# Performance work log

Measured on AMD Instinct MI355X. Metric: run time of the kernel, lower is better.

Reference implementation:

```python
import jax, jax.numpy as jnp
import numpy as np

NX = 2048
NL = 20
BATCH = 512
EIGMAX = 10.0
EPS = 1e-9


def prox_cardan(eta, x):
    """Prox of u -> -eta*(log(u)+log(1-u)) at x: unique root in (0,1) of
    u^3 - (1+x)u^2 + (x-2eta)u + eta = 0 (Cardano / trigonometric method)."""
    b = -(1.0 + x)
    c = x - 2.0 * eta
    d = eta
    p = c - b * b / 3.0
    q = 2.0 * b ** 3 / 27.0 - b * c / 3.0 + d
    disc = -4.0 * p ** 3 - 27.0 * q ** 2
    # three-real-roots branch (trigonometric); requires p<0
    pm = jnp.minimum(p, -1e-12)
    m = 2.0 * jnp.sqrt(-pm / 3.0)
    arg = jnp.clip(3.0 * q / (pm * m), -1.0, 1.0)
    th = jnp.arccos(arg)
    k = jnp.arange(3, dtype=x.dtype)
    t_trig = m[..., None] * jnp.cos((th[..., None] - 2.0 * jnp.pi * k) / 3.0)
    r_trig = t_trig - b[..., None] / 3.0
    in01 = (r_trig > 0.0) & (r_trig < 1.0)
    idx = jnp.argmax(in01, axis=-1)
    root3 = jnp.take_along_axis(r_trig, idx[..., None], axis=-1)[..., 0]
    # one-real-root branch
    s = jnp.sqrt(jnp.maximum(q * q / 4.0 + p ** 3 / 27.0, 0.0))
    root1 = jnp.cbrt(-q / 2.0 + s) + jnp.cbrt(-q / 2.0 - s) - b / 3.0
    u = jnp.where(disc >= 0.0, root3, root1)
    return jnp.clip(u, EPS, 1.0 - EPS)


def setup_inputs() -> dict:
    key = jax.random.key(0)
    k1, k2, k3, k4, k5 = jax.random.split(key, 5)
    x = jax.random.uniform(k1, (BATCH, 1, NX), dtype=jnp.float32)
    # symmetric PSD operators for T^T T and D^T D (as in a discretized inverse problem)
    A = jax.random.normal(k2, (NX, NX), dtype=jnp.float32)
    tTT = (A @ A.T) / NX
    B = jax.random.normal(k3, (NX, NX), dtype=jnp.float32)
    tDD = (B @ B.T) / NX
    # orthogonal change-of-basis: element <-> eigen bases
    Q, _ = jnp.linalg.qr(jax.random.normal(k4, (NX, NX), dtype=jnp.float32))
    Pelt = Q.astype(jnp.float32)
    Peig = Q.T.astype(jnp.float32)
    x_b = jnp.einsum('ij,bcj->bci', tTT, x) + 0.01 * jax.random.normal(k5, (BATCH, 1, NX), dtype=jnp.float32)
    gamma = jnp.full((NL,), 0.1, dtype=jnp.float32)   # nn.Parameter([0.1])
    mu = jnp.zeros((NL,), dtype=jnp.float32)          # nn.Parameter([0.0])
    reg = jnp.full((NL,), 0.001, dtype=jnp.float32)   # noisy=True -> trainable 0.001
    return {"x": x, "x_b": x_b, "tDD": tDD, "tTT": tTT, "Peig": Peig,
            "Pelt": Pelt, "gamma": gamma, "mu": mu, "reg": reg}


def reference(x, x_b, tDD, tTT, Peig, Pelt, gamma, mu, reg):
    def step(xc, params):
        g_raw, mu_raw, reg_raw = params
        g = jax.nn.softplus(g_raw)
        mu_l = jax.nn.softplus(mu_raw) / 1e6
        reg_l = jax.nn.softplus(reg_raw) / (EIGMAX ** 2)
        grad = (jnp.einsum('ij,bcj->bci', tTT, xc) - x_b
                + reg_l * jnp.einsum('ij,bcj->bci', tDD, xc))
        xt = xc - g * grad
        xt = jnp.einsum('ij,bcj->bci', Pelt, xt)
        xt = prox_cardan(g * mu_l, xt)
        xt = jnp.einsum('ij,bcj->bci', Peig, xt)
        return xt, None

    out, _ = jax.lax.scan(step, x, (gamma, mu, reg))
    return out
```

## Files before the change

### kernel.cpp

```cpp
#include <hip/hip_runtime.h>
#include <math.h>

#define MDIM 512
#define NDIM 2048
#define KDIM 2048
#define NLAYERS 20

static const size_t MN = (size_t)MDIM * NDIM;
static const size_t OPN = (size_t)KDIM * KDIM;

using bf16x8 = __attribute__((ext_vector_type(8))) short;
using f32x4  = __attribute__((ext_vector_type(4))) float;

__device__ __forceinline__ double softplusd(double v) {
    return (v > 20.0) ? v : log1p(exp(v));
}

__device__ __forceinline__ float prox_cardan_f(float eta, float x) {
    const float b  = -(1.0f + x);
    const float c  = x - 2.0f * eta;
    const float dd = eta;
    const float p  = c - b * b * (1.0f / 3.0f);
    const float q  = 2.0f * b * b * b * (1.0f / 27.0f) - b * c * (1.0f / 3.0f) + dd;
    const float disc = -4.0f * p * p * p - 27.0f * q * q;
    const float pm = fminf(p, -1e-12f);
    const float mm = 2.0f * sqrtf(-pm * (1.0f / 3.0f));
    float arg = 3.0f * q / (pm * mm);
    arg = fminf(fmaxf(arg, -1.0f), 1.0f);
    const float th = acosf(arg);
    const float TWO_PI = 6.28318530717958647692f;
    const float r0 = mm * cosf(th * (1.0f / 3.0f)) - b * (1.0f / 3.0f);
    const float r1 = mm * cosf((th - TWO_PI) * (1.0f / 3.0f)) - b * (1.0f / 3.0f);
    const float r2 = mm * cosf((th - 2.0f * TWO_PI) * (1.0f / 3.0f)) - b * (1.0f / 3.0f);
    const bool in0 = (r0 > 0.0f) && (r0 < 1.0f);
    const bool in1 = (r1 > 0.0f) && (r1 < 1.0f);
    const bool in2 = (r2 > 0.0f) && (r2 < 1.0f);
    const float root3 = in0 ? r0 : (in1 ? r1 : (in2 ? r2 : r0));
    const float s = sqrtf(fmaxf(q * q * 0.25f + p * p * p * (1.0f / 27.0f), 0.0f));
    const float root1 = cbrtf(-q * 0.5f + s) + cbrtf(-q * 0.5f - s) - b * (1.0f / 3.0f);
    const float u = (disc >= 0.0f) ? root3 : root1;
    return fminf(fmaxf(u, 1e-9f), 1.0f - 1e-9f);
}

__device__ __forceinline__ double prox_newton_d(double eta, double x) {
    double u = (double)prox_cardan_f((float)eta, (float)x);
#pragma unroll
    for (int i = 0; i < 4; ++i) {
        const double um1 = u - 1.0;
        const double umx = u - x;
        const double P  = u * um1 * umx - eta * (2.0 * u - 1.0);
        const double dP = um1 * umx + u * umx + u * um1 - 2.0 * eta;
        u = u - P / dP;
        u = fmin(fmax(u, 1e-12), 1.0 - 1e-12);
    }
    return fmin(fmax(u, 1e-9), 1.0 - 1e-9);
}

__device__ __forceinline__ unsigned short f2bf(float f) {
    unsigned u = __float_as_uint(f);
    unsigned r = (u + 0x7FFFu + ((u >> 16) & 1u)) >> 16;
    return (unsigned short)r;
}
__device__ __forceinline__ float bf2f(unsigned short h) {
    return __uint_as_float(((unsigned)h) << 16);
}
__device__ __forceinline__ void split3f(float f, unsigned short& b1,
                                        unsigned short& b2, unsigned short& b3) {
    b1 = f2bf(f);
    const float r1 = f - bf2f(b1);
    b2 = f2bf(r1);
    const float r2 = r1 - bf2f(b2);
    b3 = f2bf(r2);
}

__device__ __forceinline__ void gl16(const void* g, void* l) {
    __builtin_amdgcn_global_load_lds(
        (const __attribute__((address_space(1))) unsigned int*)g,
        (__attribute__((address_space(3))) unsigned int*)l, 16, 0, 0);
}

__global__ __launch_bounds__(256) void split3_op(
    const float* __restrict__ s1, const float* __restrict__ s2,
    const float* __restrict__ greg, int layer,
    unsigned short* __restrict__ p1, unsigned short* __restrict__ p2,
    unsigned short* __restrict__ p3) {
    const size_t i = ((size_t)blockIdx.x * 256 + threadIdx.x) * 4;
    float reglf = 0.0f;
    if (s2) reglf = (float)(softplusd((double)greg[layer]) * 0.01);
    const float4 a = *(const float4*)(s1 + i);
    float4 b = make_float4(0.f, 0.f, 0.f, 0.f);
    if (s2) b = *(const float4*)(s2 + i);
    ushort4 o1, o2, o3;
    split3f(fmaf(reglf, b.x, a.x), o1.x, o2.x, o3.x);
    split3f(fmaf(reglf, b.y, a.y), o1.y, o2.y, o3.y);
    split3f(fmaf(reglf, b.z, a.z), o1.z, o2.z, o3.z);
    split3f(fmaf(reglf, b.w, a.w), o1.w, o2.w, o3.w);
    *(ushort4*)(p1 + i) = o1;
    *(ushort4*)(p2 + i) = o2;
    *(ushort4*)(p3 + i) = o3;
}

__global__ __launch_bounds__(256) void split3_w(
    const float* __restrict__ s1, const float* __restrict__ s2,
    const float* __restrict__ greg, int layer,
    unsigned short* __restrict__ p1, unsigned short* __restrict__ p2,
    unsigned short* __restrict__ p3) {
    if (layer > 0 && greg[layer] == greg[0]) return;
    const size_t i = ((size_t)blockIdx.x * 256 + threadIdx.x) * 4;
    const float reglf = (float)(softplusd((double)greg[layer]) * 0.01);
    const float4 a = *(const float4*)(s1 + i);
    const float4 b = *(const float4*)(s2 + i);
    ushort4 o1, o2, o3;
    split3f(fmaf(reglf, b.x, a.x), o1.x, o2.x, o3.x);
    split3f(fmaf(reglf, b.y, a.y), o1.y, o2.y, o3.y);
    split3f(fmaf(reglf, b.z, a.z), o1.z, o2.z, o3.z);
    split3f(fmaf(reglf, b.w, a.w), o1.w, o2.w, o3.w);
    *(ushort4*)(p1 + i) = o1;
    *(ushort4*)(p2 + i) = o2;
    *(ushort4*)(p3 + i) = o3;
}

__global__ __launch_bounds__(256, 2) void gemm_bf16x3(
    const unsigned short* __restrict__ A1, const unsigned short* __restrict__ A2,
    const unsigned short* __restrict__ A3,
    const unsigned short* __restrict__ W1, const unsigned short* __restrict__ W2,
    const unsigned short* __restrict__ W3,
    float* __restrict__ Part, int klen, int S) {
    __shared__ __align__(16) unsigned short Ab[3][3][64][32];
    __shared__ __align__(16) unsigned short Wb[3][3][64][32];

    const int tid = threadIdx.x;

    const int nwg = 256 * S;
    const int cpx = nwg >> 3;
    const int bid = blockIdx.x;
    const int g   = (bid & 7) * cpx + (bid >> 3);
    const int xs  = g / (8 * S);
    const int rr  = g - xs * (8 * S);
    const int ys  = rr & 7;
    const int zs  = rr >> 3;
    const int n0 = xs * 64;
    const int m0 = ys * 64;
    const int kb = zs * klen;

    const int lane = tid & 63, wid = tid >> 6;
    const int quad = lane >> 4, lrow = lane & 15;
    const int wm = (wid >> 1) * 32, wn = (wid & 1) * 32;

    const int srow = tid >> 2;
    const int lc8  = ((tid & 3) ^ ((tid >> 3) & 3)) * 8;
    const int t8   = tid * 8;
    const int qx   = (quad ^ ((lrow >> 1) & 3)) * 8;

    const unsigned short* gA1 = A1 + (size_t)(m0 + srow) * KDIM + kb + lc8;
    const unsigned short* gA2 = A2 + (size_t)(m0 + srow) * KDIM + kb + lc8;
    const unsigned short* gA3 = A3 + (size_t)(m0 + srow) * KDIM + kb + lc8;
    const unsigned short* gW1 = W1 + (size_t)(n0 + srow) * KDIM + kb + lc8;
    const unsigned short* gW2 = W2 + (size_t)(n0 + srow) * KDIM + kb + lc8;
    const unsigned short* gW3 = W3 + (size_t)(n0 + srow) * KDIM + kb + lc8;

    unsigned short* lA = &Ab[0][0][0][0];
    unsigned short* lW = &Wb[0][0][0][0];

    f32x4 ahi[2][2], alo[2][2];
#pragma unroll
    for (int a = 0; a < 2; ++a)
#pragma unroll
        for (int b = 0; b < 2; ++b) {
            ahi[a][b] = (f32x4){0.f, 0.f, 0.f, 0.f};
            alo[a][b] = (f32x4){0.f, 0.f, 0.f, 0.f};
        }

    auto stage = [&](int buf, int step) {
        const int off = buf * 6144;
        const int ko  = step * 32;
        gl16(gA1 + ko, lA + off + t8);
        gl16(gA2 + ko, lA + off + 2048 + t8);
        gl16(gA3 + ko, lA + off + 4096 + t8);
        gl16(gW1 + ko, lW + off + t8);
        gl16(gW2 + ko, lW + off + 2048 + t8);
        gl16(gW3 + ko, lW + off + 4096 + t8);
    };

    const int nsteps = klen >> 5;

    stage(0, 0);
    if (nsteps > 1) stage(1, 1);

    int idx = 0;
    for (int s = 0; s < nsteps; ++s) {
        if (s + 1 < nsteps) {
            asm volatile("s_waitcnt vmcnt(6)" ::: "memory");
        } else {
            asm volatile("s_waitcnt vmcnt(0)" ::: "memory");
        }
        __builtin_amdgcn_s_barrier();
        __builtin_amdgcn_sched_barrier(0);

        if (s + 2 < nsteps) {
            int pre = idx + 2; if (pre >= 3) pre -= 3;
            stage(pre, s + 2);
        }

        const unsigned short* cA = lA + idx * 6144;
        const unsigned short* cW = lW + idx * 6144;

        bf16x8 fa[2][3], fw[2][3];
#pragma unroll
        for (int t = 0; t < 2; ++t) {
            const int ra = (wm + t * 16 + lrow) * 32;
            const int rw = (wn + t * 16 + lrow) * 32;
            fa[t][0] = *(const bf16x8*)(cA + ra + qx);
            fa[t][1] = *(const bf16x8*)(cA + 2048 + ra + qx);
            fa[t][2] = *(const bf16x8*)(cA + 4096 + ra + qx);
            fw[t][0] = *(const bf16x8*)(cW + rw + qx);
            fw[t][1] = *(const bf16x8*)(cW + 2048 + rw + qx);
            fw[t][2] = *(const bf16x8*)(cW + 4096 + rw + qx);
        }
        __builtin_amdgcn_s_setprio(1);
#pragma unroll
        for (int tm = 0; tm < 2; ++tm)
#pragma unroll
            for (int tn = 0; tn < 2; ++tn) {
                ahi[tm][tn] = __builtin_amdgcn_mfma_f32_16x16x32_bf16(fa[tm][0], fw[tn][0], ahi[tm][tn], 0, 0, 0);
                alo[tm][tn] = __builtin_amdgcn_mfma_f32_16x16x32_bf16(fa[tm][0], fw[tn][1], alo[tm][tn], 0, 0, 0);
                alo[tm][tn] = __builtin_amdgcn_mfma_f32_16x16x32_bf16(fa[tm][1], fw[tn][0], alo[tm][tn], 0, 0, 0);
                alo[tm][tn] = __builtin_amdgcn_mfma_f32_16x16x32_bf16(fa[tm][1], fw[tn][1], alo[tm][tn], 0, 0, 0);
                alo[tm][tn] = __builtin_amdgcn_mfma_f32_16x16x32_bf16(fa[tm][0], fw[tn][2], alo[tm][tn], 0, 0, 0);
                alo[tm][tn] = __builtin_amdgcn_mfma_f32_16x16x32_bf16(fa[tm][2], fw[tn][0], alo[tm][tn], 0, 0, 0);
            }
        __builtin_amdgcn_s_setprio(0);

        ++idx; if (idx == 3) idx = 0;
    }

    float* P = Part + (size_t)zs * MN;
#pragma unroll
    for (int tm = 0; tm < 2; ++tm)
#pragma unroll
        for (int tn = 0; tn < 2; ++tn) {
            const int mbase = m0 + wm + tm * 16 + quad * 4;
            const int nn = n0 + wn + tn * 16 + lrow;
#pragma unroll
            for (int r = 0; r < 4; ++r)
                P[(size_t)(mbase + r) * NDIM + nn] = ahi[tm][tn][r] + alo[tm][tn][r];
        }
}

template <int MODE>
__global__ __launch_bounds__(256) void combine3(
    const float* __restrict__ Part, int S,
    const float* __restrict__ Xc, const float* __restrict__ Xb,
    float* __restrict__ stateOut,
    unsigned short* __restrict__ p1, unsigned short* __restrict__ p2,
    unsigned short* __restrict__ p3,
    const float* __restrict__ gam, const float* __restrict__ gmu,
    const float* __restrict__ greg, int layer) {
    const size_t i = ((size_t)blockIdx.x * 256 + threadIdx.x) * 4;
    double s0 = 0.0, s1 = 0.0, s2 = 0.0, s3 = 0.0;
    for (int z = 0; z < S; ++z) {
        const float4 p = *(const float4*)(Part + (size_t)z * MN + i);
        s0 += (double)p.x; s1 += (double)p.y; s2 += (double)p.z; s3 += (double)p.w;
    }
    float v0, v1, v2, v3;
    if (MODE == 0) {
        const double g = softplusd((double)gam[layer]);
        const float4 xc = *(const float4*)(Xc + i);
        const float4 xb = *(const float4*)(Xb + i);
        v0 = (float)((double)xc.x - g * (s0 - (double)xb.x));
        v1 = (float)((double)xc.y - g * (s1 - (double)xb.y));
        v2 = (float)((double)xc.z - g * (s2 - (double)xb.z));
        v3 = (float)((double)xc.w - g * (s3 - (double)xb.w));
    } else if (MODE == 1) {
        const double g   = softplusd((double)gam[layer]);
        const double eta = g * softplusd((double)gmu[layer]) * 1e-6;
        v0 = (float)prox_newton_d(eta, s0);
        v1 = (float)prox_newton_d(eta, s1);
        v2 = (float)prox_newton_d(eta, s2);
        v3 = (float)prox_newton_d(eta, s3);
    } else {
        v0 = (float)s0; v1 = (float)s1; v2 = (float)s2; v3 = (float)s3;
        *(float4*)(stateOut + i) = make_float4(v0, v1, v2, v3);
    }
    ushort4 o1, o2, o3;
    split3f(v0, o1.x, o2.x, o3.x);
    split3f(v1, o1.y, o2.y, o3.y);
    split3f(v2, o1.z, o2.z, o3.z);
    split3f(v3, o1.w, o2.w, o3.w);
    *(ushort4*)(p1 + i) = o1;
    *(ushort4*)(p2 + i) = o2;
    *(ushort4*)(p3 + i) = o3;
}

#define BM 64
#define BN 64
#define BK 32
#define LDSP 68

__device__ __forceinline__ double prox_cardan_d(double eta, double x) {
    const double b  = -(1.0 + x);
    const double c  = x - 2.0 * eta;
    const double dd = eta;
    const double p  = c - b * b * (1.0 / 3.0);
    const double q  = 2.0 * b * b * b * (1.0 / 27.0) - b * c * (1.0 / 3.0) + dd;
    const double disc = -4.0 * p * p * p - 27.0 * q * q;
    const double pm = fmin(p, -1e-12);
    const double mm = 2.0 * sqrt(-pm * (1.0 / 3.0));
    double arg = 3.0 * q / (pm * mm);
    arg = fmin(fmax(arg, -1.0), 1.0);
    const double th = acos(arg);
    const double TWO_PI = 6.283185307179586476925286766559;
    const double r0 = mm * cos(th * (1.0 / 3.0)) - b * (1.0 / 3.0);
    const double r1 = mm * cos((th - TWO_PI) * (1.0 / 3.0)) - b * (1.0 / 3.0);
    const double r2 = mm * cos((th - 2.0 * TWO_PI) * (1.0 / 3.0)) - b * (1.0 / 3.0);
    const bool in0 = (r0 > 0.0) && (r0 < 1.0);
    const bool in1 = (r1 > 0.0) && (r1 < 1.0);
    const bool in2 = (r2 > 0.0) && (r2 < 1.0);
    const double root3 = in0 ? r0 : (in1 ? r1 : (in2 ? r2 : r0));
    const double s = sqrt(fmax(q * q * 0.25 + p * p * p * (1.0 / 27.0), 0.0));
    const double root1 = cbrt(-q * 0.5 + s) + cbrt(-q * 0.5 - s) - b * (1.0 / 3.0);
    const double u = (disc >= 0.0) ? root3 : root1;
    return fmin(fmax(u, 1e-9), 1.0 - 1e-9);
}

template <bool FUSE2>
__global__ __launch_bounds__(256, 4) void gemm_nt_splitk(
    const float* __restrict__ A, const float* __restrict__ W1,
    const float* __restrict__ W2, double* __restrict__ Part,
    const float* __restrict__ greg, int layer, int klen) {
    __shared__ float As[BK][LDSP];
    __shared__ float Ws[BK][LDSP];
    const int tid = threadIdx.x;
    const int m0 = blockIdx.y * BM;
    const int n0 = blockIdx.x * BN;
    const int kbase = blockIdx.z * klen;
    float reglf = 0.0f;
    if (FUSE2) reglf = (float)(softplusd((double)greg[layer]) * 0.01);
    const int lrow = tid >> 3;
    const int lkc  = (tid & 7) << 2;
    const float* pA  = A  + (size_t)(m0 + lrow) * KDIM + kbase + lkc;
    const float* pW  = W1 + (size_t)(n0 + lrow) * KDIM + kbase + lkc;
    const float* pW2 = FUSE2 ? (W2 + (size_t)(n0 + lrow) * KDIM + kbase + lkc) : nullptr;
    float4 ra[2], rw[2];
    ra[0] = *(const float4*)(pA);
    ra[1] = *(const float4*)(pA + 32 * KDIM);
    rw[0] = *(const float4*)(pW);
    rw[1] = *(const float4*)(pW + 32 * KDIM);
    if (FUSE2) {
        const float4 u0 = *(const float4*)(pW2);
        const float4 u1 = *(const float4*)(pW2 + 32 * KDIM);
        rw[0].x += reglf * u0.x; rw[0].y += reglf * u0.y;
        rw[0].z += reglf * u0.z; rw[0].w += reglf * u0.w;
        rw[1].x += reglf * u1.x; rw[1].y += reglf * u1.y;
        rw[1].z += reglf * u1.z; rw[1].w += reglf * u1.w;
    }
    float  acc[4][4]   = {};
    double acc64[4][4] = {};
    const int tx = (tid & 15) << 2;
    const int ty = (tid >> 4) << 2;
    int it = 0;
    for (int k0 = 0; k0 < klen; k0 += BK, ++it) {
#pragma unroll
        for (int h = 0; h < 2; ++h) {
            const int row = lrow + (h << 5);
            As[lkc + 0][row] = (h ? ra[1].x : ra[0].x);
            As[lkc + 1][row] = (h ? ra[1].y : ra[0].y);
            As[lkc + 2][row] = (h ? ra[1].z : ra[0].z);
            As[lkc + 3][row] = (h ? ra[1].w : ra[0].w);
            Ws[lkc + 0][row] = (h ? rw[1].x : rw[0].x);
            Ws[lkc + 1][row] = (h ? rw[1].y : rw[0].y);
            Ws[lkc + 2][row] = (h ? rw[1].z : rw[0].z);
            Ws[lkc + 3][row] = (h ? rw[1].w : rw[0].w);
        }
        __syncthreads();
        if (k0 + BK < klen) {
            const float* qA = pA + k0 + BK;
            ra[0] = *(const float4*)(qA);
            ra[1] = *(const float4*)(qA + 32 * KDIM);
            const float* qW = pW + k0 + BK;
            rw[0] = *(const float4*)(qW);
            rw[1] = *(const float4*)(qW + 32 * KDIM);
            if (FUSE2) {
                const float* qW2 = pW2 + k0 + BK;
                const float4 u0 = *(const float4*)(qW2);
                const float4 u1 = *(const float4*)(qW2 + 32 * KDIM);
                rw[0].x += reglf * u0.x; rw[0].y += reglf * u0.y;
                rw[0].z += reglf * u0.z; rw[0].w += reglf * u0.w;
                rw[1].x += reglf * u1.x; rw[1].y += reglf * u1.y;
                rw[1].z += reglf * u1.z; rw[1].w += reglf * u1.w;
            }
        }
#pragma unroll
        for (int kk = 0; kk < BK; ++kk) {
            const float4 a4 = *(const float4*)(&As[kk][ty]);
            const float4 b4 = *(const float4*)(&Ws[kk][tx]);
            const float av[4] = {a4.x, a4.y, a4.z, a4.w};
            const float bv[4] = {b4.x, b4.y, b4.z, b4.w};
#pragma unroll
            for (int r = 0; r < 4; ++r)
#pragma unroll
                for (int cc = 0; cc < 4; ++cc)
                    acc[r][cc] = fmaf(av[r], bv[cc], acc[r][cc]);
        }
        __syncthreads();
        if ((it & 1) == 1) {
#pragma unroll
            for (int r = 0; r < 4; ++r)
#pragma unroll
                for (int cc = 0; cc < 4; ++cc) {
                    acc64[r][cc] += (double)acc[r][cc];
                    acc[r][cc] = 0.0f;
                }
        }
    }
#pragma unroll
    for (int r = 0; r < 4; ++r)
#pragma unroll
        for (int cc = 0; cc < 4; ++cc)
            acc64[r][cc] += (double)acc[r][cc];
    double* Pz = Part + (size_t)blockIdx.z * MN;
#pragma unroll
    for (int r = 0; r < 4; ++r) {
        double* q = Pz + (size_t)(m0 + ty + r) * NDIM + n0 + tx;
        *(double2*)(q)     = make_double2(acc64[r][0], acc64[r][1]);
        *(double2*)(q + 2) = make_double2(acc64[r][2], acc64[r][3]);
    }
}

template <int MODE>
__global__ __launch_bounds__(256) void combine_ep(
    const double* __restrict__ Part, int nslices,
    const float* __restrict__ Xc, const float* __restrict__ Xb,
    float* __restrict__ Out,
    const float* __restrict__ gam, const float* __restrict__ gmu,
    const float* __restrict__ greg, int layer) {
    const size_t i4 = ((size_t)blockIdx.x * 256 + threadIdx.x) * 4;
    double s0 = 0.0, s1 = 0.0, s2 = 0.0, s3 = 0.0;
    for (int z = 0; z < nslices; ++z) {
        const double* p = Part + (size_t)z * MN + i4;
        const double2 a = *(const double2*)(p);
        const double2 b = *(const double2*)(p + 2);
        s0 += a.x; s1 += a.y; s2 += b.x; s3 += b.y;
    }
    float4 o;
    if (MODE == 0) {
        const double g = softplusd((double)gam[layer]);
        const float4 xc = *(const float4*)(Xc + i4);
        const float4 xb = *(const float4*)(Xb + i4);
        o.x = (float)((double)xc.x - g * (s0 - (double)xb.x));
        o.y = (float)((double)xc.y - g * (s1 - (double)xb.y));
        o.z = (float)((double)xc.z - g * (s2 - (double)xb.z));
        o.w = (float)((double)xc.w - g * (s3 - (double)xb.w));
    } else if (MODE == 1) {
        const double g   = softplusd((double)gam[layer]);
        const double eta = g * softplusd((double)gmu[layer]) * 1e-6;
        o.x = (float)prox_cardan_d(eta, s0);
        o.y = (float)prox_cardan_d(eta, s1);
        o.z = (float)prox_cardan_d(eta, s2);
        o.w = (float)prox_cardan_d(eta, s3);
    } else {
        o.x = (float)s0; o.y = (float)s1; o.z = (float)s2; o.w = (float)s3;
    }
    *(float4*)(Out + i4) = o;
}

extern "C" void kernel_launch(void* const* d_in, const int* in_sizes, int n_in,
                              void* d_out, int out_size, void* d_ws, size_t ws_size,
                              hipStream_t stream) {
    const float* x    = (const float*)d_in[0];
    const float* x_b  = (const float*)d_in[1];
    const float* tDD  = (const float*)d_in[2];
    const float* tTT  = (const float*)d_in[3];
    const float* Peig = (const float*)d_in[4];
    const float* Pelt = (const float*)d_in[5];
    const float* gam  = (const float*)d_in[6];
    const float* gmu  = (const float*)d_in[7];
    const float* greg = (const float*)d_in[8];
    float* out = (float*)d_out;

    const size_t TRI_OP_B = 3 * OPN * 2;
    const size_t TRI_A_B  = 3 * MN * 2;
    const size_t STATE_B  = MN * 4;
    const size_t full_need = 3 * TRI_OP_B + 2 * TRI_A_B + STATE_B + 2 * MN * 4;
    const size_t mid_need  = 1 * TRI_OP_B + 2 * TRI_A_B + STATE_B + 2 * MN * 4;

    const bool full = (ws_size >= full_need);
    const bool mid  = (!full && ws_size >= mid_need);

    if (full || mid) {
        const int S = 2;
        const int klen = KDIM / S;
        char* p = (char*)d_ws;
        unsigned short *Wt1, *Wt2, *Wt3, *Pe1, *Pe2, *Pe3, *Pg1, *Pg2, *Pg3;
        if (full) {
            Wt1 = (unsigned short*)p;        Wt2 = Wt1 + OPN; Wt3 = Wt2 + OPN; p += TRI_OP_B;
            Pe1 = (unsigned short*)p;        Pe2 = Pe1 + OPN; Pe3 = Pe2 + OPN; p += TRI_OP_B;
            Pg1 = (unsigned short*)p;        Pg2 = Pg1 + OPN; Pg3 = Pg2 + OPN; p += TRI_OP_B;
        } else {
            Wt1 = (unsigned short*)p;        Wt2 = Wt1 + OPN; Wt3 = Wt2 + OPN; p += TRI_OP_B;
            Pe1 = Wt1; Pe2 = Wt2; Pe3 = Wt3;
            Pg1 = Wt1; Pg2 = Wt2; Pg3 = Wt3;
        }
        unsigned short* Aa1 = (unsigned short*)p; unsigned short* Aa2 = Aa1 + MN;
        unsigned short* Aa3 = Aa2 + MN; p += TRI_A_B;
        unsigned short* Ab1 = (unsigned short*)p; unsigned short* Ab2 = Ab1 + MN;
        unsigned short* Ab3 = Ab2 + MN; p += TRI_A_B;
        float* state = (float*)p; p += STATE_B;
        float* part  = (float*)p;

        const dim3 gg((unsigned)(256 * S));
        const unsigned cgrid = (unsigned)(MN / 4 / 256);
        const unsigned ogrid = (unsigned)(OPN / 4 / 256);

        split3_op<<<cgrid, 256, 0, stream>>>(x, nullptr, greg, 0, Aa1, Aa2, Aa3);
        if (full) {
            split3_op<<<ogrid, 256, 0, stream>>>(Pelt, nullptr, greg, 0, Pe1, Pe2, Pe3);
            split3_op<<<ogrid, 256, 0, stream>>>(Peig, nullptr, greg, 0, Pg1, Pg2, Pg3);
        }

        unsigned short *c1 = Aa1, *c2 = Aa2, *c3 = Aa3;
        unsigned short *d1 = Ab1, *d2 = Ab2, *d3 = Ab3;

        for (int l = 0; l < NLAYERS; ++l) {
            if (full) {
                split3_w<<<ogrid, 256, 0, stream>>>(tTT, tDD, greg, l, Wt1, Wt2, Wt3);
            } else {
                split3_op<<<ogrid, 256, 0, stream>>>(tTT, tDD, greg, l, Wt1, Wt2, Wt3);
            }
            gemm_bf16x3<<<gg, 256, 0, stream>>>(c1, c2, c3, Wt1, Wt2, Wt3, part, klen, S);
            combine3<0><<<cgrid, 256, 0, stream>>>(part, S, (l == 0 ? x : state), x_b,
                                                   nullptr, d1, d2, d3, gam, gmu, greg, l);
            if (mid) split3_op<<<ogrid, 256, 0, stream>>>(Pelt, nullptr, greg, 0, Pe1, Pe2, Pe3);
            gemm_bf16x3<<<gg, 256, 0, stream>>>(d1, d2, d3, Pe1, Pe2, Pe3, part, klen, S);
            combine3<1><<<cgrid, 256, 0, stream>>>(part, S, nullptr, nullptr,
                                                   nullptr, c1, c2, c3, gam, gmu, greg, l);
            if (mid) split3_op<<<ogrid, 256, 0, stream>>>(Peig, nullptr, greg, 0, Pg1, Pg2, Pg3);
            gemm_bf16x3<<<gg, 256, 0, stream>>>(c1, c2, c3, Pg1, Pg2, Pg3, part, klen, S);
            combine3<2><<<cgrid, 256, 0, stream>>>(part, S, nullptr, nullptr,
                                                   (l == NLAYERS - 1 ? out : state),
                                                   d1, d2, d3, gam, gmu, greg, l);
            unsigned short* t;
            t = c1; c1 = d1; d1 = t;
            t = c2; c2 = d2; d2 = t;
            t = c3; c3 = d3; d3 = t;
        }
        return;
    }

    char* wsb = (char*)d_ws;
    float* b0 = (float*)wsb;
    float* b1 = b0 + MN;
    float* b2 = b1 + MN;
    float* b3 = b2 + MN;
    const size_t base_bytes = 4 * MN * sizeof(float);
    double* partd = (double*)(wsb + base_bytes);
    int S = 0;
    if (ws_size >= base_bytes + 2 * MN * sizeof(double)) S = 2;
    else if (ws_size >= base_bytes + 1 * MN * sizeof(double)) S = 1;
    if (S == 0) return;
    const int klen = KDIM / S;
    dim3 gg(NDIM / BN, MDIM / BM, S);
    dim3 cg((unsigned)(MN / 4 / 256));
    const float* cur = x;
    float* bx = b0; float* bu = b1; float* bn = b2; float* bo = b3;
    for (int l = 0; l < NLAYERS; ++l) {
        gemm_nt_splitk<true><<<gg, 256, 0, stream>>>(cur, tTT, tDD, partd, greg, l, klen);
        combine_ep<0><<<cg, 256, 0, stream>>>(partd, S, cur, x_b, bx, gam, gmu, greg, l);
        gemm_nt_splitk<false><<<gg, 256, 0, stream>>>(bx, Pelt, nullptr, partd, greg, l, klen);
        combine_ep<1><<<cg, 256, 0, stream>>>(partd, S, nullptr, nullptr, bu, gam, gmu, greg, l);
        gemm_nt_splitk<false><<<gg, 256, 0, stream>>>(bu, Peig, nullptr, partd, greg, l, klen);
        float* dst = (l == NLAYERS - 1) ? out : bn;
        combine_ep<2><<<cg, 256, 0, stream>>>(partd, S, nullptr, nullptr, dst, gam, gmu, greg, l);
        cur = bn;
        float* t = bn; bn = bo; bo = t;
    }
}
```

Measured before the change: 2.719 ms.

## Pre-tile activations into MFMA fragment layout and load A directly to registers

The activation split kernels and combine kernels now write the bf16x3 activation pieces in a fragment-tiled layout matching the MFMA operand order. The GEMM then loads A fragments straight from global memory into registers, double-buffered across steps, instead of staging them through LDS. Each wave stages only its own W rows into a per-wave LDS buffer, which removes the block-wide barrier. The MFMA issue order is also regrouped by component. This cuts LDS traffic and synchronisation but makes each wave rely on global-load latency hiding for A, and it duplicates A fetches across the two waves sharing an m-tile.

Result: slower. 3.026 ms (+11.3%).

```diff
diff --git a/kernel.cpp b/kernel.cpp
--- a/kernel.cpp
+++ b/kernel.cpp
@@ -79,6 +79,7 @@
         (__attribute__((address_space(3))) unsigned int*)l, 16, 0, 0);
 }
 
+
 __global__ __launch_bounds__(256) void split3_op(
     const float* __restrict__ s1, const float* __restrict__ s2,
     const float* __restrict__ greg, int layer,
@@ -120,14 +121,38 @@
     *(ushort4*)(p3 + i) = o3;
 }
 
+__global__ __launch_bounds__(256) void split3_a(
+    const float* __restrict__ src,
+    unsigned short* __restrict__ p1, unsigned short* __restrict__ p2,
+    unsigned short* __restrict__ p3) {
+    const int b = blockIdx.x;
+    const int wid = threadIdx.x >> 6, lane = threadIdx.x & 63;
+    const int msub = b >> 4, kblk = (b & 15) * 4 + wid;
+    const int m = msub * 16 + (lane & 15);
+    const int n = kblk * 32 + (lane >> 4) * 8;
+    const size_t flat = (size_t)m * NDIM + n;
+    const size_t tile = ((size_t)(msub * 64 + kblk) * 64 + lane) * 8;
+    const float4 a = *(const float4*)(src + flat);
+    const float4 c = *(const float4*)(src + flat + 4);
+    const float v[8] = {a.x, a.y, a.z, a.w, c.x, c.y, c.z, c.w};
+    unsigned short o1[8], o2[8], o3[8];
+#pragma unroll
+    for (int j = 0; j < 8; ++j) split3f(v[j], o1[j], o2[j], o3[j]);
+    *(ushort4*)(p1 + tile)     = make_ushort4(o1[0], o1[1], o1[2], o1[3]);
+    *(ushort4*)(p1 + tile + 4) = make_ushort4(o1[4], o1[5], o1[6], o1[7]);
+    *(ushort4*)(p2 + tile)     = make_ushort4(o2[0], o2[1], o2[2], o2[3]);
+    *(ushort4*)(p2 + tile + 4) = make_ushort4(o2[4], o2[5], o2[6], o2[7]);
+    *(ushort4*)(p3 + tile)     = make_ushort4(o3[0], o3[1], o3[2], o3[3]);
+    *(ushort4*)(p3 + tile + 4) = make_ushort4(o3[4], o3[5], o3[6], o3[7]);
+}
+
 __global__ __launch_bounds__(256, 2) void gemm_bf16x3(
     const unsigned short* __restrict__ A1, const unsigned short* __restrict__ A2,
     const unsigned short* __restrict__ A3,
     const unsigned short* __restrict__ W1, const unsigned short* __restrict__ W2,
     const unsigned short* __restrict__ W3,
     float* __restrict__ Part, int klen, int S) {
-    __shared__ __align__(16) unsigned short Ab[3][3][64][32];
-    __shared__ __align__(16) unsigned short Wb[3][3][64][32];
+    __shared__ __align__(16) unsigned short Wb[4][3][3][1024];
 
     const int tid = threadIdx.x;
 
@@ -140,100 +165,131 @@
     const int ys  = rr & 7;
     const int zs  = rr >> 3;
     const int n0 = xs * 64;
-    const int m0 = ys * 64;
     const int kb = zs * klen;
 
     const int lane = tid & 63, wid = tid >> 6;
     const int quad = lane >> 4, lrow = lane & 15;
     const int wm = (wid >> 1) * 32, wn = (wid & 1) * 32;
-
-    const int srow = tid >> 2;
-    const int lc8  = ((tid & 3) ^ ((tid >> 3) & 3)) * 8;
-    const int t8   = tid * 8;
-    const int qx   = (quad ^ ((lrow >> 1) & 3)) * 8;
-
-    const unsigned short* gA1 = A1 + (size_t)(m0 + srow) * KDIM + kb + lc8;
-    const unsigned short* gA2 = A2 + (size_t)(m0 + srow) * KDIM + kb + lc8;
-    const unsigned short* gA3 = A3 + (size_t)(m0 + srow) * KDIM + kb + lc8;
-    const unsigned short* gW1 = W1 + (size_t)(n0 + srow) * KDIM + kb + lc8;
-    const unsigned short* gW2 = W2 + (size_t)(n0 + srow) * KDIM + kb + lc8;
-    const unsigned short* gW3 = W3 + (size_t)(n0 + srow) * KDIM + kb + lc8;
-
-    unsigned short* lA = &Ab[0][0][0][0];
-    unsigned short* lW = &Wb[0][0][0][0];
+    const int swq = (quad ^ ((lrow >> 1) & 3)) * 8;
+
+    const int nsteps = klen >> 5;
+    const int kblk0  = zs * nsteps;
+
+    const unsigned short* pAb[2][3];
+#pragma unroll
+    for (int t = 0; t < 2; ++t) {
+        const int msubA = ys * 4 + (wid >> 1) * 2 + t;
+        const size_t base = ((size_t)(msubA * 64 + kblk0) * 64 + lane) * 8;
+        pAb[t][0] = A1 + base;
+        pAb[t][1] = A2 + base;
+        pAb[t][2] = A3 + base;
+    }
+
+    const int lc8 = ((lane & 3) ^ ((lane >> 3) & 3)) * 8;
+    const size_t wrow = (size_t)(n0 + wn + (lane >> 2)) * KDIM + kb + lc8;
+    const unsigned short* gWs[3] = {W1 + wrow, W2 + wrow, W3 + wrow};
+
+    unsigned short* wbase = &Wb[wid][0][0][0];
 
     f32x4 ahi[2][2], alo[2][2];
 #pragma unroll
     for (int a = 0; a < 2; ++a)
 #pragma unroll
-        for (int b = 0; b < 2; ++b) {
-            ahi[a][b] = (f32x4){0.f, 0.f, 0.f, 0.f};
-            alo[a][b] = (f32x4){0.f, 0.f, 0.f, 0.f};
-        }
-
-    auto stage = [&](int buf, int step) {
-        const int off = buf * 6144;
-        const int ko  = step * 32;
-        gl16(gA1 + ko, lA + off + t8);
-        gl16(gA2 + ko, lA + off + 2048 + t8);
-        gl16(gA3 + ko, lA + off + 4096 + t8);
-        gl16(gW1 + ko, lW + off + t8);
-        gl16(gW2 + ko, lW + off + 2048 + t8);
-        gl16(gW3 + ko, lW + off + 4096 + t8);
-    };
-
-    const int nsteps = klen >> 5;
-
-    stage(0, 0);
-    if (nsteps > 1) stage(1, 1);
-
-    int idx = 0;
-    for (int s = 0; s < nsteps; ++s) {
+        for (int b2 = 0; b2 < 2; ++b2) {
+            ahi[a][b2] = (f32x4){0.f, 0.f, 0.f, 0.f};
+            alo[a][b2] = (f32x4){0.f, 0.f, 0.f, 0.f};
+        }
+
+    bf16x8 faA[2][3], faB[2][3];
+
+#pragma unroll
+    for (int st = 0; st < 2; ++st)
+#pragma unroll
+        for (int p = 0; p < 3; ++p)
+#pragma unroll
+            for (int h = 0; h < 2; ++h)
+                gl16(gWs[p] + (size_t)h * 32768 + st * 32,
+                     wbase + st * 3072 + p * 1024 + h * 512);
+#pragma unroll
+    for (int t = 0; t < 2; ++t)
+#pragma unroll
+        for (int p = 0; p < 3; ++p)
+            faA[t][p] = *(const bf16x8*)(pAb[t][p]);
+    asm volatile("s_waitcnt vmcnt(0)" ::: "memory");
+    __builtin_amdgcn_sched_barrier(0);
+
+    auto STEP = [&](bf16x8 (&cur)[2][3], bf16x8 (&nxt)[2][3], int s) {
         if (s + 1 < nsteps) {
             asm volatile("s_waitcnt vmcnt(6)" ::: "memory");
         } else {
             asm volatile("s_waitcnt vmcnt(0)" ::: "memory");
         }
-        __builtin_amdgcn_s_barrier();
         __builtin_amdgcn_sched_barrier(0);
-
+        if (s + 1 < nsteps) {
+#pragma unroll
+            for (int t = 0; t < 2; ++t)
+#pragma unroll
+                for (int p = 0; p < 3; ++p)
+                    nxt[t][p] = *(const bf16x8*)(pAb[t][p] + (size_t)(s + 1) * 512);
+        }
         if (s + 2 < nsteps) {
-            int pre = idx + 2; if (pre >= 3) pre -= 3;
-            stage(pre, s + 2);
-        }
-
-        const unsigned short* cA = lA + idx * 6144;
-        const unsigned short* cW = lW + idx * 6144;
-
-        bf16x8 fa[2][3], fw[2][3];
+            const int bu = (s + 2) % 3;
+#pragma unroll
+            for (int p = 0; p < 3; ++p)
+#pragma unroll
+                for (int h = 0; h < 2; ++h)
+                    gl16(gWs[p] + (size_t)h * 32768 + (s + 2) * 32,
+                         wbase + bu * 3072 + p * 1024 + h * 512);
+        }
+        const int bc = s % 3;
+        bf16x8 fw[2][3];
 #pragma unroll
         for (int t = 0; t < 2; ++t) {
-            const int ra = (wm + t * 16 + lrow) * 32;
-            const int rw = (wn + t * 16 + lrow) * 32;
-            fa[t][0] = *(const bf16x8*)(cA + ra + qx);
-            fa[t][1] = *(const bf16x8*)(cA + 2048 + ra + qx);
-            fa[t][2] = *(const bf16x8*)(cA + 4096 + ra + qx);
-            fw[t][0] = *(const bf16x8*)(cW + rw + qx);
-            fw[t][1] = *(const bf16x8*)(cW + 2048 + rw + qx);
-            fw[t][2] = *(const bf16x8*)(cW + 4096 + rw + qx);
+            const int roff = (t * 16 + lrow) * 32 + swq;
+#pragma unroll
+            for (int p = 0; p < 3; ++p)
+                fw[t][p] = *(const bf16x8*)(wbase + bc * 3072 + p * 1024 + roff);
         }
         __builtin_amdgcn_s_setprio(1);
 #pragma unroll
         for (int tm = 0; tm < 2; ++tm)
 #pragma unroll
-            for (int tn = 0; tn < 2; ++tn) {
-                ahi[tm][tn] = __builtin_amdgcn_mfma_f32_16x16x32_bf16(fa[tm][0], fw[tn][0], ahi[tm][tn], 0, 0, 0);
-                alo[tm][tn] = __builtin_amdgcn_mfma_f32_16x16x32_bf16(fa[tm][0], fw[tn][1], alo[tm][tn], 0, 0, 0);
-                alo[tm][tn] = __builtin_amdgcn_mfma_f32_16x16x32_bf16(fa[tm][1], fw[tn][0], alo[tm][tn], 0, 0, 0);
-                alo[tm][tn] = __builtin_amdgcn_mfma_f32_16x16x32_bf16(fa[tm][1], fw[tn][1], alo[tm][tn], 0, 0, 0);
-                alo[tm][tn] = __builtin_amdgcn_mfma_f32_16x16x32_bf16(fa[tm][0], fw[tn][2], alo[tm][tn], 0, 0, 0);
-                alo[tm][tn] = __builtin_amdgcn_mfma_f32_16x16x32_bf16(fa[tm][2], fw[tn][0], alo[tm][tn], 0, 0, 0);
-            }
+            for (int tn = 0; tn < 2; ++tn)
+                ahi[tm][tn] = __builtin_amdgcn_mfma_f32_16x16x32_bf16(cur[tm][0], fw[tn][0], ahi[tm][tn], 0, 0, 0);
+#pragma unroll
+        for (int tm = 0; tm < 2; ++tm)
+#pragma unroll
+            for (int tn = 0; tn < 2; ++tn)
+                alo[tm][tn] = __builtin_amdgcn_mfma_f32_16x16x32_bf16(cur[tm][0], fw[tn][1], alo[tm][tn], 0, 0, 0);
+#pragma unroll
+        for (int tm = 0; tm < 2; ++tm)
+#pragma unroll
+            for (int tn = 0; tn < 2; ++tn)
+                alo[tm][tn] = __builtin_amdgcn_mfma_f32_16x16x32_bf16(cur[tm][1], fw[tn][0], alo[tm][tn], 0, 0, 0);
+#pragma unroll
+        for (int tm = 0; tm < 2; ++tm)
+#pragma unroll
+            for (int tn = 0; tn < 2; ++tn)
+                alo[tm][tn] = __builtin_amdgcn_mfma_f32_16x16x32_bf16(cur[tm][1], fw[tn][1], alo[tm][tn], 0, 0, 0);
+#pragma unroll
+        for (int tm = 0; tm < 2; ++tm)
+#pragma unroll
+            for (int tn = 0; tn < 2; ++tn)
+                alo[tm][tn] = __builtin_amdgcn_mfma_f32_16x16x32_bf16(cur[tm][0], fw[tn][2], alo[tm][tn], 0, 0, 0);
+#pragma unroll
+        for (int tm = 0; tm < 2; ++tm)
+#pragma unroll
+            for (int tn = 0; tn < 2; ++tn)
+                alo[tm][tn] = __builtin_amdgcn_mfma_f32_16x16x32_bf16(cur[tm][2], fw[tn][0], alo[tm][tn], 0, 0, 0);
         __builtin_amdgcn_s_setprio(0);
-
-        ++idx; if (idx == 3) idx = 0;
-    }
-
+    };
+
+    for (int s = 0; s < nsteps; s += 2) {
+        STEP(faA, faB, s);
+        STEP(faB, faA, s + 1);
+    }
+
+    const int m0 = ys * 64;
     float* P = Part + (size_t)zs * MN;
 #pragma unroll
     for (int tm = 0; tm < 2; ++tm)
@@ -256,40 +312,54 @@
     unsigned short* __restrict__ p3,
     const float* __restrict__ gam, const float* __restrict__ gmu,
     const float* __restrict__ greg, int layer) {
-    const size_t i = ((size_t)blockIdx.x * 256 + threadIdx.x) * 4;
-    double s0 = 0.0, s1 = 0.0, s2 = 0.0, s3 = 0.0;
+    const int b = blockIdx.x;
+    const int wid = threadIdx.x >> 6, lane = threadIdx.x & 63;
+    const int msub = b >> 4, kblk = (b & 15) * 4 + wid;
+    const int m = msub * 16 + (lane & 15);
+    const int n = kblk * 32 + (lane >> 4) * 8;
+    const size_t flat = (size_t)m * NDIM + n;
+    const size_t tile = ((size_t)(msub * 64 + kblk) * 64 + lane) * 8;
+
+    double s[8] = {0., 0., 0., 0., 0., 0., 0., 0.};
     for (int z = 0; z < S; ++z) {
-        const float4 p = *(const float4*)(Part + (size_t)z * MN + i);
-        s0 += (double)p.x; s1 += (double)p.y; s2 += (double)p.z; s3 += (double)p.w;
-    }
-    float v0, v1, v2, v3;
+        const float4 a = *(const float4*)(Part + (size_t)z * MN + flat);
+        const float4 c = *(const float4*)(Part + (size_t)z * MN + flat + 4);
+        s[0] += (double)a.x; s[1] += (double)a.y; s[2] += (double)a.z; s[3] += (double)a.w;
+        s[4] += (double)c.x; s[5] += (double)c.y; s[6] += (double)c.z; s[7] += (double)c.w;
+    }
+    float v[8];
     if (MODE == 0) {
         const double g = softplusd((double)gam[layer]);
-        const float4 xc = *(const float4*)(Xc + i);
-        const float4 xb = *(const float4*)(Xb + i);
-        v0 = (float)((double)xc.x - g * (s0 - (double)xb.x));
-        v1 = (float)((double)xc.y - g * (s1 - (double)xb.y));
-        v2 = (float)((double)xc.z - g * (s2 - (double)xb.z));
-        v3 = (float)((double)xc.w - g * (s3 - (double)xb.w));
+        const float4 xa = *(const float4*)(Xc + flat);
+        const float4 xc = *(const float4*)(Xc + flat + 4);
+        const float4 ba = *(const float4*)(Xb + flat);
+        const float4 bc = *(const float4*)(Xb + flat + 4);
+        const float xcv[8] = {xa.x, xa.y, xa.z, xa.w, xc.x, xc.y, xc.z, xc.w};
+        const float xbv[8] = {ba.x, ba.y, ba.z, ba.w, bc.x, bc.y, bc.z, bc.w};
+#pragma unroll
+        for (int j = 0; j < 8; ++j)
+            v[j] = (float)((double)xcv[j] - g * (s[j] - (double)xbv[j]));
     } else if (MODE == 1) {
         const double g   = softplusd((double)gam[layer]);
         const double eta = g * softplusd((double)gmu[layer]) * 1e-6;
-        v0 = (float)prox_newton_d(eta, s0);
-        v1 = (float)prox_newton_d(eta, s1);
-        v2 = (float)prox_newton_d(eta, s2);
-        v3 = (float)prox_newton_d(eta, s3);
+#pragma unroll
+        for (int j = 0; j < 8; ++j)
+            v[j] = (float)prox_newton_d(eta, s[j]);
     } else {
-        v0 = (float)s0; v1 = (float)s1; v2 = (float)s2; v3 = (float)s3;
-        *(float4*)(stateOut + i) = make_float4(v0, v1, v2, v3);
-    }
-    ushort4 o1, o2, o3;
-    split3f(v0, o1.x, o2.x, o3.x);
-    split3f(v1, o1.y, o2.y, o3.y);
-    split3f(v2, o1.z, o2.z, o3.z);
-    split3f(v3, o1.w, o2.w, o3.w);
-    *(ushort4*)(p1 + i) = o1;
-    *(ushort4*)(p2 + i) = o2;
-    *(ushort4*)(p3 + i) = o3;
+#pragma unroll
+        for (int j = 0; j < 8; ++j) v[j] = (float)s[j];
+        *(float4*)(stateOut + flat)     = make_float4(v[0], v[1], v[2], v[3]);
+        *(float4*)(stateOut + flat + 4) = make_float4(v[4], v[5], v[6], v[7]);
+    }
+    unsigned short o1[8], o2[8], o3[8];
+#pragma unroll
+    for (int j = 0; j < 8; ++j) split3f(v[j], o1[j], o2[j], o3[j]);
+    *(ushort4*)(p1 + tile)     = make_ushort4(o1[0], o1[1], o1[2], o1[3]);
+    *(ushort4*)(p1 + tile + 4) = make_ushort4(o1[4], o1[5], o1[6], o1[7]);
+    *(ushort4*)(p2 + tile)     = make_ushort4(o2[0], o2[1], o2[2], o2[3]);
+    *(ushort4*)(p2 + tile + 4) = make_ushort4(o2[4], o2[5], o2[6], o2[7]);
+    *(ushort4*)(p3 + tile)     = make_ushort4(o3[0], o3[1], o3[2], o3[3]);
+    *(ushort4*)(p3 + tile + 4) = make_ushort4(o3[4], o3[5], o3[6], o3[7]);
 }
 
 #define BM 64
@@ -509,10 +579,10 @@
         float* part  = (float*)p;
 
         const dim3 gg((unsigned)(256 * S));
-        const unsigned cgrid = (unsigned)(MN / 4 / 256);
+        const unsigned agrid = 512;
         const unsigned ogrid = (unsigned)(OPN / 4 / 256);
 
-        split3_op<<<cgrid, 256, 0, stream>>>(x, nullptr, greg, 0, Aa1, Aa2, Aa3);
+        split3_a<<<agrid, 256, 0, stream>>>(x, Aa1, Aa2, Aa3);
         if (full) {
             split3_op<<<ogrid, 256, 0, stream>>>(Pelt, nullptr, greg, 0, Pe1, Pe2, Pe3);
             split3_op<<<ogrid, 256, 0, stream>>>(Peig, nullptr, greg, 0, Pg1, Pg2, Pg3);
@@ -528,15 +598,15 @@
                 split3_op<<<ogrid, 256, 0, stream>>>(tTT, tDD, greg, l, Wt1, Wt2, Wt3);
             }
             gemm_bf16x3<<<gg, 256, 0, stream>>>(c1, c2, c3, Wt1, Wt2, Wt3, part, klen, S);
-            combine3<0><<<cgrid, 256, 0, stream>>>(part, S, (l == 0 ? x : state), x_b,
+            combine3<0><<<agrid, 256, 0, stream>>>(part, S, (l == 0 ? x : state), x_b,
                                                    nullptr, d1, d2, d3, gam, gmu, greg, l);
             if (mid) split3_op<<<ogrid, 256, 0, stream>>>(Pelt, nullptr, greg, 0, Pe1, Pe2, Pe3);
             gemm_bf16x3<<<gg, 256, 0, stream>>>(d1, d2, d3, Pe1, Pe2, Pe3, part, klen, S);
-            combine3<1><<<cgrid, 256, 0, stream>>>(part, S, nullptr, nullptr,
+            combine3<1><<<agrid, 256, 0, stream>>>(part, S, nullptr, nullptr,
                                                    nullptr, c1, c2, c3, gam, gmu, greg, l);
             if (mid) split3_op<<<ogrid, 256, 0, stream>>>(Peig, nullptr, greg, 0, Pg1, Pg2, Pg3);
             gemm_bf16x3<<<gg, 256, 0, stream>>>(c1, c2, c3, Pg1, Pg2, Pg3, part, klen, S);
-            combine3<2><<<cgrid, 256, 0, stream>>>(part, S, nullptr, nullptr,
+            combine3<2><<<agrid, 256, 0, stream>>>(part, S, nullptr, nullptr,
                                                    (l == NLAYERS - 1 ? out : state),
                                                    d1, d2, d3, gam, gmu, greg, l);
             unsigned short* t;
```
